# Performance work log

Hardware: AMD Instinct MI355X
Metric: run time of the kernel (lower is better)

Reference implementation:

```python
import jax, jax.numpy as jnp
import numpy as np

N = 10000      # nodes
E = 160000     # edges
F_IN = 128     # input_dim
HID = 128      # hidden_dim = per-head channels (concat=False)
OUT = 128      # output_dim
H = 4          # heads
L = 4          # layers (all 128->128 here, so params stack)


def setup_inputs() -> dict:
    key = jax.random.key(0)
    ks = jax.random.split(key, 12)
    x = jax.random.normal(ks[0], (N, F_IN), dtype=jnp.float32)
    edge_index = jax.random.randint(ks[1], (2, E), 0, N, dtype=jnp.int64)
    s = 1.0 / np.sqrt(F_IN)
    Wq = jax.random.normal(ks[2], (L, F_IN, H * HID), dtype=jnp.float32) * s
    bq = jnp.zeros((L, H * HID), dtype=jnp.float32)
    Wk = jax.random.normal(ks[3], (L, F_IN, H * HID), dtype=jnp.float32) * s
    bk = jnp.zeros((L, H * HID), dtype=jnp.float32)
    Wv = jax.random.normal(ks[4], (L, F_IN, H * HID), dtype=jnp.float32) * s
    bv = jnp.zeros((L, H * HID), dtype=jnp.float32)
    Wskip = jax.random.normal(ks[5], (L, F_IN, HID), dtype=jnp.float32) * s
    bskip = jnp.zeros((L, HID), dtype=jnp.float32)
    return {"x": x, "edge_index": edge_index, "Wq": Wq, "bq": bq,
            "Wk": Wk, "bk": bk, "Wv": Wv, "bv": bv,
            "Wskip": Wskip, "bskip": bskip}


def _transformer_conv(x, src, dst, Wq, bq, Wk, bk, Wv, bv, Ws, bs):
    # PyG TransformerConv, concat=False (mean over heads), root_weight=True
    n = x.shape[0]
    q = (x @ Wq + bq).reshape(n, H, HID)
    k = (x @ Wk + bk).reshape(n, H, HID)
    v = (x @ Wv + bv).reshape(n, H, HID)
    # per-edge attention logits: [E, H]
    alpha = jnp.einsum('ehc,ehc->eh', q[dst], k[src]) / jnp.sqrt(jnp.float32(HID))
    # segment softmax over destination node
    m = jax.ops.segment_max(alpha, dst, num_segments=n)          # [N, H]
    e = jnp.exp(alpha - m[dst])                                  # [E, H]
    z = jax.ops.segment_sum(e, dst, num_segments=n)              # [N, H]
    a = e / z[dst]                                               # [E, H]
    msg = a[:, :, None] * v[src]                                 # [E, H, C]
    out = jax.ops.segment_sum(msg, dst, num_segments=n)          # [N, H, C]
    out = out.mean(axis=1)                                       # concat=False
    return out + x @ Ws + bs                                     # skip (root_weight)


def reference(x, edge_index, Wq, bq, Wk, bk, Wv, bv, Wskip, bskip):
    src = edge_index[0]
    dst = edge_index[1]
    h = x
    for l in range(L - 1):
        h = _transformer_conv(h, src, dst, Wq[l], bq[l], Wk[l], bk[l],
                              Wv[l], bv[l], Wskip[l], bskip[l])
        h = jax.nn.relu(h)  # dropout p in eval/reference is identity
    h = _transformer_conv(h, src, dst, Wq[-1], bq[-1], Wk[-1], bk[-1],
                          Wv[-1], bv[-1], Wskip[-1], bskip[-1])
    return h
```

## Files before the change

### kernel.cpp

```cpp
#include <hip/hip_runtime.h>
#include <math.h>

static constexpr int F  = 128;
static constexpr int H  = 4;
static constexpr int HF = 512;
static constexpr int NCP = 640;
static constexpr int LAYERS = 4;

typedef __attribute__((ext_vector_type(8))) short bf16x8;
typedef __attribute__((ext_vector_type(4))) float f32x4;

__device__ __forceinline__ unsigned short f2bf(float f) {
    union { float f; unsigned u; } v; v.f = f;
    unsigned r = (v.u + 0x7FFFu + ((v.u >> 16) & 1u)) >> 16;
    return (unsigned short)r;
}
__device__ __forceinline__ float bf2f(unsigned short b) {
    union { unsigned u; float f; } v; v.u = ((unsigned)b) << 16;
    return v.f;
}

__device__ __forceinline__ float row16_sum(float x) {
    int t;
    t = __builtin_amdgcn_update_dpp(0, __float_as_int(x), 0xB1, 0xF, 0xF, true);
    x += __int_as_float(t);
    t = __builtin_amdgcn_update_dpp(0, __float_as_int(x), 0x4E, 0xF, 0xF, true);
    x += __int_as_float(t);
    t = __builtin_amdgcn_update_dpp(0, __float_as_int(x), 0x124, 0xF, 0xF, true);
    x += __int_as_float(t);
    t = __builtin_amdgcn_update_dpp(0, __float_as_int(x), 0x128, 0xF, 0xF, true);
    x += __int_as_float(t);
    return x;
}

__global__ void zero_kernel(int* __restrict__ p, int n) {
    int i = blockIdx.x * blockDim.x + threadIdx.x;
    if (i < n) p[i] = 0;
}

__global__ void hist_kernel(const int* __restrict__ dst, int* __restrict__ deg, int E) {
    int e = blockIdx.x * blockDim.x + threadIdx.x;
    if (e < E) atomicAdd(&deg[dst[e]], 1);
}

__global__ void scan_kernel(const int* __restrict__ deg, int* __restrict__ row_ptr, int n) {
    __shared__ int wsum[16];
    __shared__ int carry_s, wtot_s;
    const int tid = threadIdx.x;
    const int lane = tid & 63;
    const int wid = tid >> 6;
    if (tid == 0) { carry_s = 0; row_ptr[0] = 0; }
    __syncthreads();
    for (int base = 0; base < n; base += 1024) {
        int i = base + tid;
        int x = (i < n) ? deg[i] : 0;
#pragma unroll
        for (int off = 1; off < 64; off <<= 1) {
            int t = __shfl_up(x, off, 64);
            if (lane >= off) x += t;
        }
        if (lane == 63) wsum[wid] = x;
        __syncthreads();
        if (tid == 0) {
            int s = 0;
#pragma unroll
            for (int j = 0; j < 16; ++j) { int t = wsum[j]; wsum[j] = s; s += t; }
            wtot_s = s;
        }
        __syncthreads();
        int incl = x + wsum[wid] + carry_s;
        if (i < n) row_ptr[i + 1] = incl;
        __syncthreads();
        if (tid == 0) carry_s += wtot_s;
        __syncthreads();
    }
}

__global__ void scatter_kernel(const int* __restrict__ src, const int* __restrict__ dst,
                               const int* __restrict__ row_ptr, int* __restrict__ cursor,
                               int* __restrict__ csr_src, int E) {
    int e = blockIdx.x * blockDim.x + threadIdx.x;
    if (e < E) {
        int d = dst[e];
        int pos = atomicAdd(&cursor[d], 1);
        csr_src[row_ptr[d] + pos] = src[e];
    }
}

static constexpr int NB_CONV  = 1250;
static constexpr int NB_WQK   = 64;
static constexpr int NB_WS    = 64;
static constexpr int NB_BPOST = 256;
static constexpr int NB_BIAS  = LAYERS;
static constexpr int NB_PREP  = NB_CONV + NB_WQK + NB_WS + NB_BPOST + NB_BIAS;

__global__ __launch_bounds__(256) void prep_kernel(
    const float* __restrict__ x, unsigned short* __restrict__ h_bf, int n4,
    const float* __restrict__ Wq, const float* __restrict__ Wk,
    const float* __restrict__ Wv, const float* __restrict__ Ws,
    const float* __restrict__ bq, const float* __restrict__ bs, const float* __restrict__ bv,
    unsigned short* __restrict__ Bpre, unsigned short* __restrict__ Bpost,
    float* __restrict__ biasPre, float* __restrict__ biasPost, float scale)
{
    __shared__ __attribute__((aligned(16))) float smem[64 * 33 * 2];
    const int tid = threadIdx.x;
    int b = blockIdx.x;

    if (b < NB_CONV) {
        int i = b * 256 + tid;
        if (i < n4) {
            float4 v = *(const float4*)(x + (size_t)i * 4);
            ushort4 o;
            o.x = f2bf(v.x); o.y = f2bf(v.y); o.z = f2bf(v.z); o.w = f2bf(v.w);
            *(ushort4*)(h_bf + (size_t)i * 4) = o;
        }
        return;
    }
    b -= NB_CONV;
    if (b < NB_WQK) {
        float (*As)[33] = (float (*)[33])smem;
        float (*Bs)[33] = (float (*)[33])(smem + 64 * 33);
        const int bx = b & 1, by = (b >> 1) & 1, lh = b >> 2;
        const int l = lh >> 2, h = lh & 3;
        const int c0 = by * 64, k0 = bx * 64;
        const float* Ab = Wk + (size_t)l * 65536 + h * 128;
        const float* Bb = Wq + (size_t)l * 65536 + h * 128;
        const int tx = tid & 15, ty = tid >> 4;
        float acc[4][4] = {};
        for (int jj = 0; jj < 128; jj += 32) {
#pragma unroll
            for (int rep = 0; rep < 2; ++rep) {
                int f = tid + rep * 256;
                int r = f >> 3, j4 = (f & 7) * 4;
                float4 a = *(const float4*)(Ab + (size_t)(c0 + r) * 512 + jj + j4);
                As[r][j4 + 0] = a.x; As[r][j4 + 1] = a.y; As[r][j4 + 2] = a.z; As[r][j4 + 3] = a.w;
                float4 bb = *(const float4*)(Bb + (size_t)(k0 + r) * 512 + jj + j4);
                Bs[r][j4 + 0] = bb.x; Bs[r][j4 + 1] = bb.y; Bs[r][j4 + 2] = bb.z; Bs[r][j4 + 3] = bb.w;
            }
            __syncthreads();
#pragma unroll
            for (int j = 0; j < 32; ++j) {
                float a0 = As[ty * 4 + 0][j], a1 = As[ty * 4 + 1][j];
                float a2 = As[ty * 4 + 2][j], a3 = As[ty * 4 + 3][j];
                float b0 = Bs[tx * 4 + 0][j], b1 = Bs[tx * 4 + 1][j];
                float b2 = Bs[tx * 4 + 2][j], b3 = Bs[tx * 4 + 3][j];
                acc[0][0] += a0 * b0; acc[0][1] += a0 * b1; acc[0][2] += a0 * b2; acc[0][3] += a0 * b3;
                acc[1][0] += a1 * b0; acc[1][1] += a1 * b1; acc[1][2] += a1 * b2; acc[1][3] += a1 * b3;
                acc[2][0] += a2 * b0; acc[2][1] += a2 * b1; acc[2][2] += a2 * b2; acc[2][3] += a2 * b3;
                acc[3][0] += a3 * b0; acc[3][1] += a3 * b1; acc[3][2] += a3 * b2; acc[3][3] += a3 * b3;
            }
            __syncthreads();
        }
#pragma unroll
        for (int i = 0; i < 4; ++i)
#pragma unroll
            for (int t = 0; t < 4; ++t) {
                int c = c0 + ty * 4 + i;
                int k = k0 + tx * 4 + t;
                Bpre[(size_t)l * NCP * 128 + (size_t)(h * 128 + c) * 128 + k] = f2bf(scale * acc[i][t]);
            }
        return;
    }
    b -= NB_WQK;
    if (b < NB_WS) {
        unsigned short (*t)[33] = (unsigned short (*)[33])smem;
        const int bx = b & 3, by = (b >> 2) & 3, l = b >> 4;
        const int k0 = bx * 32, n0 = by * 32;
        const int cx = tid & 31, ry = tid >> 5;
#pragma unroll
        for (int rr = 0; rr < 32; rr += 8) {
            int k = k0 + ry + rr;
            t[ry + rr][cx] = f2bf(Ws[(size_t)l * 16384 + (size_t)k * 128 + n0 + cx]);
        }
        __syncthreads();
#pragma unroll
        for (int rr = 0; rr < 32; rr += 8) {
            int n = n0 + ry + rr;
            Bpre[(size_t)l * NCP * 128 + (size_t)(512 + n) * 128 + k0 + cx] = t[cx][ry + rr];
        }
        return;
    }
    b -= NB_WS;
    if (b < NB_BPOST) {
        unsigned short (*t)[33] = (unsigned short (*)[33])smem;
        const int bx = b & 3, by = (b >> 2) & 3, lh = b >> 4;
        const int l = lh >> 2, h = lh & 3;
        const int ci0 = bx * 32, co0 = by * 32;
        const int cx = tid & 31, ry = tid >> 5;
#pragma unroll
        for (int rr = 0; rr < 32; rr += 8) {
            int ci = ci0 + ry + rr;
            t[ry + rr][cx] = f2bf(0.25f * Wv[(size_t)l * 65536 + (size_t)ci * 512 + h * 128 + co0 + cx]);
        }
        __syncthreads();
#pragma unroll
        for (int rr = 0; rr < 32; rr += 8) {
            int co = co0 + ry + rr;
            Bpost[(size_t)l * 65536 + (size_t)co * 512 + h * 128 + ci0 + cx] = t[cx][ry + rr];
        }
        return;
    }
    b -= NB_BPOST;
    {
        const int l = b;
        for (int n = tid; n < 512; n += 256) {
            int h = n >> 7, c = n & 127;
            float s = 0.f;
            for (int j = 0; j < 128; ++j)
                s += bq[(size_t)l * 512 + h * 128 + j] * Wk[(size_t)l * 65536 + (size_t)c * 512 + h * 128 + j];
            biasPre[(size_t)l * NCP + n] = s * scale;
        }
        for (int c = tid; c < 128; c += 256) {
            float s = 0.f;
            for (int h = 0; h < 4; ++h) s += bv[(size_t)l * 512 + h * 128 + c];
            biasPost[(size_t)l * 128 + c] = 0.25f * s + bs[(size_t)l * 128 + c];
        }
    }
}

__global__ __launch_bounds__(256) void gemm_pre(
    const unsigned short* __restrict__ Abf,
    const unsigned short* __restrict__ Bt,
    const float* __restrict__ bias,
    unsigned short* __restrict__ Qt,
    int M)
{
    __shared__ unsigned short As[128][72];
    __shared__ unsigned short Bs[128][72];

    const int tid = threadIdx.x;
    const int wave = tid >> 6, lane = tid & 63;
    const int lane16 = lane & 15, quad = lane >> 4;
    const int wr = wave >> 1, wc = wave & 1;
    const int row0 = blockIdx.y * 128;
    const int col0 = blockIdx.x * 128;

    f32x4 acc[4][4] = {};

    for (int kk = 0; kk < 128; kk += 64) {
#pragma unroll
        for (int j = 0; j < 4; ++j) {
            int c = tid + j * 256;
            int r = c >> 3, c8 = (c & 7) * 8;
            bf16x8 v = {};
            if (row0 + r < M) v = *(const bf16x8*)(Abf + (size_t)(row0 + r) * 128 + kk + c8);
            *(bf16x8*)&As[r][c8] = v;
        }
#pragma unroll
        for (int j = 0; j < 4; ++j) {
            int c = tid + j * 256;
            int r = c >> 3, c8 = (c & 7) * 8;
            *(bf16x8*)&Bs[r][c8] = *(const bf16x8*)(Bt + (size_t)(col0 + r) * 128 + kk + c8);
        }
        __syncthreads();

#pragma unroll
        for (int ks = 0; ks < 2; ++ks) {
            bf16x8 a[4], b[4];
#pragma unroll
            for (int i = 0; i < 4; ++i)
                a[i] = *(const bf16x8*)&As[wr * 64 + i * 16 + lane16][ks * 32 + quad * 8];
#pragma unroll
            for (int i = 0; i < 4; ++i)
                b[i] = *(const bf16x8*)&Bs[wc * 64 + i * 16 + lane16][ks * 32 + quad * 8];
#pragma unroll
            for (int mi = 0; mi < 4; ++mi)
#pragma unroll
                for (int ni = 0; ni < 4; ++ni)
                    acc[mi][ni] = __builtin_amdgcn_mfma_f32_16x16x32_bf16(
                        a[mi], b[ni], acc[mi][ni], 0, 0, 0);
        }
        __syncthreads();
    }

#pragma unroll
    for (int mi = 0; mi < 4; ++mi) {
        int rowb = row0 + wr * 64 + mi * 16 + quad * 4;
#pragma unroll
        for (int ni = 0; ni < 4; ++ni) {
            int col = col0 + wc * 64 + ni * 16 + lane16;
            float bv = bias[col];
#pragma unroll
            for (int r = 0; r < 4; ++r) {
                int gr = rowb + r;
                if (gr < M) Qt[(size_t)gr * 512 + col] = f2bf(acc[mi][ni][r] + bv);
            }
        }
    }
}

__global__ __launch_bounds__(128, 4) void attn_agg(
    const unsigned short* __restrict__ Qt,
    const unsigned short* __restrict__ Hb,
    const int* __restrict__ row_ptr,
    const int* __restrict__ csr_src,
    unsigned short* __restrict__ Agg,
    int N)
{
    __shared__ float part[4][16][10];

    const int tid = threadIdx.x;
    const int wv  = tid >> 6;
    const int g   = (tid >> 4) & 3;
    const int l16 = tid & 15;
    const int node = blockIdx.x;

    const float NEG = -3e38f;

    float qf[8];
    {
        bf16x8 qv = *(const bf16x8*)(Qt + (size_t)node * HF + g * F + l16 * 8);
#pragma unroll
        for (int j = 0; j < 8; ++j) qf[j] = bf2f((unsigned short)qv[j]);
    }
    const unsigned short* Hl = Hb + (size_t)l16 * 8;

    const int beg = row_ptr[node];
    const int end = row_ptr[node + 1];

    float m = NEG, z = 0.f;
    float acc[8];
#pragma unroll
    for (int j = 0; j < 8; ++j) acc[j] = 0.f;

    const int begw = beg + wv * 4;
    if (begw < end) {
        const int last = end - 1;
        const int NB = (end - begw + 7) >> 3;

#define CLD(i) csr_src[(i) < last ? (i) : last]

        int a0 = CLD(begw + 0), a1 = CLD(begw + 1), a2 = CLD(begw + 2), a3 = CLD(begw + 3);
        bf16x8 hA0 = *(const bf16x8*)(Hl + (size_t)a0 * F);
        bf16x8 hA1 = *(const bf16x8*)(Hl + (size_t)a1 * F);
        bf16x8 hA2 = *(const bf16x8*)(Hl + (size_t)a2 * F);
        bf16x8 hA3 = *(const bf16x8*)(Hl + (size_t)a3 * F);
        int b0 = CLD(begw + 8), b1 = CLD(begw + 9), b2 = CLD(begw + 10), b3 = CLD(begw + 11);
        bf16x8 hB0 = *(const bf16x8*)(Hl + (size_t)b0 * F);
        bf16x8 hB1 = *(const bf16x8*)(Hl + (size_t)b1 * F);
        bf16x8 hB2 = *(const bf16x8*)(Hl + (size_t)b2 * F);
        bf16x8 hB3 = *(const bf16x8*)(Hl + (size_t)b3 * F);
        a0 = CLD(begw + 16); a1 = CLD(begw + 17); a2 = CLD(begw + 18); a3 = CLD(begw + 19);
        b0 = CLD(begw + 24); b1 = CLD(begw + 25); b2 = CLD(begw + 26); b3 = CLD(begw + 27);
        __builtin_amdgcn_sched_barrier(0);

#define ATTN_BATCH(H0, H1, H2, H3, I0, I1, I2, I3)                              \
    {                                                                           \
        float hf[4][8];                                                         \
        _Pragma("unroll")                                                       \
        for (int j = 0; j < 8; ++j) {                                           \
            hf[0][j] = bf2f((unsigned short)H0[j]);                             \
            hf[1][j] = bf2f((unsigned short)H1[j]);                             \
            hf[2][j] = bf2f((unsigned short)H2[j]);                             \
            hf[3][j] = bf2f((unsigned short)H3[j]);                             \
        }                                                                       \
        if (k + 2 < NB) {                                                       \
            H0 = *(const bf16x8*)(Hl + (size_t)I0 * F);                         \
            H1 = *(const bf16x8*)(Hl + (size_t)I1 * F);                         \
            H2 = *(const bf16x8*)(Hl + (size_t)I2 * F);                         \
            H3 = *(const bf16x8*)(Hl + (size_t)I3 * F);                         \
            I0 = CLD(base + 32); I1 = CLD(base + 33);                           \
            I2 = CLD(base + 34); I3 = CLD(base + 35);                           \
        }                                                                       \
        __builtin_amdgcn_sched_barrier(0);   \
        float p0 = 0.f, p1 = 0.f, p2 = 0.f, p3 = 0.f;                           \
        _Pragma("unroll")                                                       \
        for (int j = 0; j < 8; ++j) {                                           \
            p0 += qf[j] * hf[0][j]; p1 += qf[j] * hf[1][j];                     \
            p2 += qf[j] * hf[2][j]; p3 += qf[j] * hf[3][j];                     \
        }                                                                       \
        p0 = row16_sum(p0); p1 = row16_sum(p1);                                 \
        p2 = row16_sum(p2); p3 = row16_sum(p3);                                 \
        const int nv = end - base;                                              \
        if (nv < 4) { if (nv < 2) p1 = NEG; if (nv < 3) p2 = NEG; p3 = NEG; }   \
        float bm = fmaxf(fmaxf(p0, p1), fmaxf(p2, p3));                         \
        float mn = fmaxf(m, bm);                                                \
        float rs = exp2f(m - mn);                                               \
        float w0 = exp2f(p0 - mn), w1 = exp2f(p1 - mn);                         \
        float w2 = exp2f(p2 - mn), w3 = exp2f(p3 - mn);                         \
        z = z * rs + (w0 + w1) + (w2 + w3);                                     \
        _Pragma("unroll")                                                       \
        for (int j = 0; j < 8; ++j)                                             \
            acc[j] = acc[j] * rs + w0 * hf[0][j] + w1 * hf[1][j]                \
                   + w2 * hf[2][j] + w3 * hf[3][j];                             \
        m = mn;                                                                 \
    }

        int base = begw;
        int k = 0;
        for (;;) {
            ATTN_BATCH(hA0, hA1, hA2, hA3, a0, a1, a2, a3)
            ++k; base += 8;
            if (k >= NB) break;
            ATTN_BATCH(hB0, hB1, hB2, hB3, b0, b1, b2, b3)
            ++k; base += 8;
            if (k >= NB) break;
        }
#undef ATTN_BATCH
#undef CLD
    }

    if (wv == 1) {
#pragma unroll
        for (int j = 0; j < 8; ++j) part[g][l16][j] = acc[j];
        part[g][l16][8] = m;
        part[g][l16][9] = z;
    }
    __syncthreads();
    if (wv == 0) {
        float om = part[g][l16][8];
        float oz = part[g][l16][9];
        float M  = fmaxf(m, om);
        float sa = exp2f(m - M);
        float sb = exp2f(om - M);
        float zz = z * sa + oz * sb;
        float inv = (zz > 0.f) ? 1.f / zz : 0.f;
        bf16x8 o;
#pragma unroll
        for (int j = 0; j < 8; ++j)
            o[j] = (short)f2bf((acc[j] * sa + part[g][l16][j] * sb) * inv);
        *(bf16x8*)(Agg + (size_t)node * HF + g * F + l16 * 8) = o;
    }
}

__global__ __launch_bounds__(256) void gemm_post(
    const unsigned short* __restrict__ Agg,
    const unsigned short* __restrict__ Hc,
    const unsigned short* __restrict__ Bt,
    const unsigned short* __restrict__ Bsk,
    const float* __restrict__ bias,
    float* __restrict__ out_f,
    unsigned short* __restrict__ out_bf,
    int relu, int M)
{
    __shared__ unsigned short As[64][72];
    __shared__ unsigned short Bs[64][72];

    const int tid = threadIdx.x;
    const int wave = tid >> 6, lane = tid & 63;
    const int lane16 = lane & 15, quad = lane >> 4;
    const int row0 = blockIdx.y * 64;
    const int col0 = blockIdx.x * 64;

    f32x4 acc[4] = {};

    for (int kk = 0; kk < 640; kk += 64) {
        const bool sk = kk >= 512;
        const int k0 = sk ? kk - 512 : kk;
#pragma unroll
        for (int rep = 0; rep < 2; ++rep) {
            int c = tid + rep * 256;
            int r = c >> 3, c8 = (c & 7) * 8;
            bf16x8 v = {};
            if (row0 + r < M)
                v = sk ? *(const bf16x8*)(Hc  + (size_t)(row0 + r) * 128 + k0 + c8)
                       : *(const bf16x8*)(Agg + (size_t)(row0 + r) * 512 + k0 + c8);
            *(bf16x8*)&As[r][c8] = v;
            *(bf16x8*)&Bs[r][c8] = sk
                ? *(const bf16x8*)(Bsk + (size_t)(col0 + r) * 128 + k0 + c8)
                : *(const bf16x8*)(Bt  + (size_t)(col0 + r) * 512 + k0 + c8);
        }
        __syncthreads();

#pragma unroll
        for (int ks = 0; ks < 2; ++ks) {
            bf16x8 b = *(const bf16x8*)&Bs[wave * 16 + lane16][ks * 32 + quad * 8];
#pragma unroll
            for (int mt = 0; mt < 4; ++mt) {
                bf16x8 a = *(const bf16x8*)&As[mt * 16 + lane16][ks * 32 + quad * 8];
                acc[mt] = __builtin_amdgcn_mfma_f32_16x16x32_bf16(a, b, acc[mt], 0, 0, 0);
            }
        }
        __syncthreads();
    }

    const int col = col0 + wave * 16 + lane16;
    const float bcol = bias[col];
#pragma unroll
    for (int mt = 0; mt < 4; ++mt) {
#pragma unroll
        for (int r = 0; r < 4; ++r) {
            int row = row0 + mt * 16 + quad * 4 + r;
            if (row < M) {
                float v = acc[mt][r] + bcol;
                if (relu) v = fmaxf(v, 0.f);
                if (out_f)  out_f[(size_t)row * 128 + col] = v;
                if (out_bf) out_bf[(size_t)row * 128 + col] = f2bf(v);
            }
        }
    }
}

extern "C" void kernel_launch(void* const* d_in, const int* in_sizes, int n_in,
                              void* d_out, int out_size, void* d_ws, size_t ws_size,
                              hipStream_t stream) {
    const float* x     = (const float*)d_in[0];
    const int*   ei    = (const int*)d_in[1];
    const float* Wq    = (const float*)d_in[2];
    const float* bq    = (const float*)d_in[3];
    const float* Wk    = (const float*)d_in[4];
    const float* bk    = (const float*)d_in[5];
    const float* Wv    = (const float*)d_in[6];
    const float* bv    = (const float*)d_in[7];
    const float* Wskip = (const float*)d_in[8];
    const float* bskip = (const float*)d_in[9];
    float* out = (float*)d_out;
    (void)bk;

    const int N = in_sizes[0] / F;
    const int E = in_sizes[1] / 2;
    const float scale = 0.08838834764831845f * 1.4426950408889634f;

    const int* src = ei;
    const int* dst = ei + E;

    char* p = (char*)d_ws;
    float* biasPreP = (float*)p;               p += (size_t)LAYERS * NCP * sizeof(float);
    float* biasPostP= (float*)p;               p += (size_t)LAYERS * 128 * sizeof(float);
    unsigned short* h0    = (unsigned short*)p; p += (size_t)N * F * sizeof(unsigned short);
    unsigned short* h1    = (unsigned short*)p; p += (size_t)N * F * sizeof(unsigned short);
    unsigned short* Qt    = (unsigned short*)p; p += (size_t)N * HF * sizeof(unsigned short);
    unsigned short* AggB  = (unsigned short*)p; p += (size_t)N * HF * sizeof(unsigned short);
    unsigned short* BpreP = (unsigned short*)p; p += (size_t)LAYERS * NCP * 128 * sizeof(unsigned short);
    unsigned short* BpostP= (unsigned short*)p; p += (size_t)LAYERS * 128 * 512 * sizeof(unsigned short);
    int* deg     = (int*)p;                    p += (size_t)N * sizeof(int);
    int* cursor  = (int*)p;                    p += (size_t)N * sizeof(int);
    int* row_ptr = (int*)p;                    p += (size_t)(N + 1) * sizeof(int);
    int* csr_src = (int*)p;

    {
        int blocks = (E + 255) / 256;
        int zn = 2 * N;
        zero_kernel<<<(zn + 255) / 256, 256, 0, stream>>>(deg, zn);
        hist_kernel<<<blocks, 256, 0, stream>>>(dst, deg, E);
        scan_kernel<<<1, 1024, 0, stream>>>(deg, row_ptr, N);
        scatter_kernel<<<blocks, 256, 0, stream>>>(src, dst, row_ptr, cursor, csr_src, E);
    }

    prep_kernel<<<NB_PREP, 256, 0, stream>>>(x, h0, N * F / 4,
                                             Wq, Wk, Wv, Wskip,
                                             bq, bskip, bv,
                                             BpreP, BpostP, biasPreP, biasPostP, scale);

    const int rowBlocks128 = (N + 127) / 128;
    const int rowBlocks64  = (N + 63) / 64;

    unsigned short* hcur = h0;
    unsigned short* hnxt = h1;
    for (int l = 0; l < LAYERS; ++l) {
        dim3 gridPre(4, rowBlocks128);
        gemm_pre<<<gridPre, 256, 0, stream>>>(hcur,
                                              BpreP + (size_t)l * NCP * 128,
                                              biasPreP + (size_t)l * NCP,
                                              Qt, N);

        attn_agg<<<N, 128, 0, stream>>>(Qt, hcur, row_ptr, csr_src, AggB, N);

        float* out_f = nullptr;
        unsigned short* out_bf = nullptr;
        int relu;
        if (l == LAYERS - 1) { out_f = out; relu = 0; }
        else { out_bf = hnxt; relu = 1; }

        dim3 gridPost(2, rowBlocks64);
        gemm_post<<<gridPost, 256, 0, stream>>>(AggB, hcur,
                                                BpostP + (size_t)l * 128 * 512,
                                                BpreP + (size_t)l * NCP * 128 + (size_t)512 * 128,
                                                biasPostP + (size_t)l * 128,
                                                out_f, out_bf, relu, N);

        unsigned short* t = hcur; hcur = hnxt; hnxt = t;
    }
}
```

Measured before the change: 254.5 us.

## Fuse post-aggregation GEMM with next layer's Q projection GEMM

For non-final layers, a single kernel now computes the post-aggregation GEMM (agg plus skip, with ReLU), keeps the resulting 64-row tile of hidden states in shared memory, and immediately multiplies it by the next layer's 512-column Q weights. This drops one kernel launch per layer and the re-read of the hidden states from global memory. In exchange the fused grid has only about 157 blocks, each doing serial work over four column tiles, so parallelism drops compared with the separate 2D-gridded GEMMs.

```diff
diff --git a/kernel.cpp b/kernel.cpp
--- a/kernel.cpp
+++ b/kernel.cpp
@@ -423,15 +423,136 @@
     }
 }
 
+__global__ __launch_bounds__(256) void gemm_post_pre(
+    const unsigned short* __restrict__ Agg,
+    const unsigned short* __restrict__ Hc,
+    const unsigned short* __restrict__ BtPost,
+    const unsigned short* __restrict__ Bsk,
+    const float* __restrict__ biasPost,
+    unsigned short* __restrict__ Hn,
+    const unsigned short* __restrict__ BtPre,
+    const float* __restrict__ biasPre,
+    unsigned short* __restrict__ Qt,
+    int M)
+{
+    __shared__ unsigned short As[64][72];
+    __shared__ unsigned short Bs[128][72];
+    __shared__ unsigned short Hs[64][136];
+
+    const int tid = threadIdx.x;
+    const int wave = tid >> 6, lane = tid & 63;
+    const int lane16 = lane & 15, quad = lane >> 4;
+    const int row0 = blockIdx.x * 64;
+
+    {
+        f32x4 acc[4][2] = {};
+        for (int kk = 0; kk < 640; kk += 64) {
+            const bool sk = kk >= 512;
+            const int k0 = sk ? kk - 512 : kk;
+#pragma unroll
+            for (int j = 0; j < 2; ++j) {
+                int c = tid + j * 256;
+                int r = c >> 3, c8 = (c & 7) * 8;
+                bf16x8 v = {};
+                if (row0 + r < M)
+                    v = sk ? *(const bf16x8*)(Hc  + (size_t)(row0 + r) * 128 + k0 + c8)
+                           : *(const bf16x8*)(Agg + (size_t)(row0 + r) * 512 + k0 + c8);
+                *(bf16x8*)&As[r][c8] = v;
+            }
+#pragma unroll
+            for (int j = 0; j < 4; ++j) {
+                int c = tid + j * 256;
+                int r = c >> 3, c8 = (c & 7) * 8;
+                *(bf16x8*)&Bs[r][c8] = sk
+                    ? *(const bf16x8*)(Bsk    + (size_t)r * 128 + k0 + c8)
+                    : *(const bf16x8*)(BtPost + (size_t)r * 512 + k0 + c8);
+            }
+            __syncthreads();
+#pragma unroll
+            for (int ks = 0; ks < 2; ++ks) {
+                bf16x8 b[2];
+#pragma unroll
+                for (int ni = 0; ni < 2; ++ni)
+                    b[ni] = *(const bf16x8*)&Bs[wave * 32 + ni * 16 + lane16][ks * 32 + quad * 8];
+#pragma unroll
+                for (int mi = 0; mi < 4; ++mi) {
+                    bf16x8 a = *(const bf16x8*)&As[mi * 16 + lane16][ks * 32 + quad * 8];
+#pragma unroll
+                    for (int ni = 0; ni < 2; ++ni)
+                        acc[mi][ni] = __builtin_amdgcn_mfma_f32_16x16x32_bf16(
+                            a, b[ni], acc[mi][ni], 0, 0, 0);
+                }
+            }
+            __syncthreads();
+        }
+#pragma unroll
+        for (int mi = 0; mi < 4; ++mi)
+#pragma unroll
+            for (int ni = 0; ni < 2; ++ni) {
+                int col = wave * 32 + ni * 16 + lane16;
+                float bcol = biasPost[col];
+#pragma unroll
+                for (int r = 0; r < 4; ++r) {
+                    int lr = mi * 16 + quad * 4 + r;
+                    unsigned short hb = f2bf(fmaxf(acc[mi][ni][r] + bcol, 0.f));
+                    Hs[lr][col] = hb;
+                    if (row0 + lr < M) Hn[(size_t)(row0 + lr) * 128 + col] = hb;
+                }
+            }
+    }
+    __syncthreads();
+
+    for (int ct = 0; ct < 4; ++ct) {
+        const int colp = ct * 128;
+        f32x4 acc2[4][2] = {};
+        for (int kk2 = 0; kk2 < 128; kk2 += 64) {
+#pragma unroll
+            for (int j = 0; j < 4; ++j) {
+                int c = tid + j * 256;
+                int r = c >> 3, c8 = (c & 7) * 8;
+                *(bf16x8*)&Bs[r][c8] =
+                    *(const bf16x8*)(BtPre + (size_t)(colp + r) * 128 + kk2 + c8);
+            }
+            __syncthreads();
+#pragma unroll
+            for (int ks = 0; ks < 2; ++ks) {
+                bf16x8 b[2];
+#pragma unroll
+                for (int ni = 0; ni < 2; ++ni)
+                    b[ni] = *(const bf16x8*)&Bs[wave * 32 + ni * 16 + lane16][ks * 32 + quad * 8];
+#pragma unroll
+                for (int mi = 0; mi < 4; ++mi) {
+                    bf16x8 a = *(const bf16x8*)&Hs[mi * 16 + lane16][kk2 + ks * 32 + quad * 8];
+#pragma unroll
+                    for (int ni = 0; ni < 2; ++ni)
+                        acc2[mi][ni] = __builtin_amdgcn_mfma_f32_16x16x32_bf16(
+                            a, b[ni], acc2[mi][ni], 0, 0, 0);
+                }
+            }
+            __syncthreads();
+        }
+#pragma unroll
+        for (int mi = 0; mi < 4; ++mi)
+#pragma unroll
+            for (int ni = 0; ni < 2; ++ni) {
+                int col = colp + wave * 32 + ni * 16 + lane16;
+                float bv = biasPre[col];
+#pragma unroll
+                for (int r = 0; r < 4; ++r) {
+                    int row = row0 + mi * 16 + quad * 4 + r;
+                    if (row < M) Qt[(size_t)row * 512 + col] = f2bf(acc2[mi][ni][r] + bv);
+                }
+            }
+    }
+}
+
 __global__ __launch_bounds__(256) void gemm_post(
     const unsigned short* __restrict__ Agg,
     const unsigned short* __restrict__ Hc,
     const unsigned short* __restrict__ Bt,
     const unsigned short* __restrict__ Bsk,
     const float* __restrict__ bias,
-    float* __restrict__ out_f,
-    unsigned short* __restrict__ out_bf,
-    int relu, int M)
+    float* __restrict__ out_f, int M)
 {
     __shared__ unsigned short As[64][72];
     __shared__ unsigned short Bs[64][72];
@@ -481,12 +602,7 @@
 #pragma unroll
         for (int r = 0; r < 4; ++r) {
             int row = row0 + mt * 16 + quad * 4 + r;
-            if (row < M) {
-                float v = acc[mt][r] + bcol;
-                if (relu) v = fmaxf(v, 0.f);
-                if (out_f)  out_f[(size_t)row * 128 + col] = v;
-                if (out_bf) out_bf[(size_t)row * 128 + col] = f2bf(v);
-            }
+            if (row < M) out_f[(size_t)row * 128 + col] = acc[mt][r] + bcol;
         }
     }
 }
@@ -547,28 +663,32 @@
 
     unsigned short* hcur = h0;
     unsigned short* hnxt = h1;
+
+    dim3 gridPre(4, rowBlocks128);
+    gemm_pre<<<gridPre, 256, 0, stream>>>(hcur, BpreP, biasPreP, Qt, N);
+
     for (int l = 0; l < LAYERS; ++l) {
-        dim3 gridPre(4, rowBlocks128);
-        gemm_pre<<<gridPre, 256, 0, stream>>>(hcur,
-                                              BpreP + (size_t)l * NCP * 128,
-                                              biasPreP + (size_t)l * NCP,
-                                              Qt, N);
-
         attn_agg<<<N, 128, 0, stream>>>(Qt, hcur, row_ptr, csr_src, AggB, N);
 
-        float* out_f = nullptr;
-        unsigned short* out_bf = nullptr;
-        int relu;
-        if (l == LAYERS - 1) { out_f = out; relu = 0; }
-        else { out_bf = hnxt; relu = 1; }
-
-        dim3 gridPost(2, rowBlocks64);
-        gemm_post<<<gridPost, 256, 0, stream>>>(AggB, hcur,
-                                                BpostP + (size_t)l * 128 * 512,
-                                                BpreP + (size_t)l * NCP * 128 + (size_t)512 * 128,
-                                                biasPostP + (size_t)l * 128,
-                                                out_f, out_bf, relu, N);
-
-        unsigned short* t = hcur; hcur = hnxt; hnxt = t;
-    }
-}
+        if (l < LAYERS - 1) {
+            gemm_post_pre<<<rowBlocks64, 256, 0, stream>>>(
+                AggB, hcur,
+                BpostP + (size_t)l * 128 * 512,
+                BpreP + (size_t)l * NCP * 128 + (size_t)512 * 128,
+                biasPostP + (size_t)l * 128,
+                hnxt,
+                BpreP + (size_t)(l + 1) * NCP * 128,
+                biasPreP + (size_t)(l + 1) * NCP,
+                Qt, N);
+            unsigned short* t = hcur; hcur = hnxt; hnxt = t;
+        } else {
+            dim3 gridPost(2, rowBlocks64);
+            gemm_post<<<gridPost, 256, 0, stream>>>(
+                AggB, hcur,
+                BpostP + (size_t)l * 128 * 512,
+                BpreP + (size_t)l * NCP * 128 + (size_t)512 * 128,
+                biasPostP + (size_t)l * 128,
+                out, N);
+        }
+    }
+}
```

Result: slower. 266.6 us (+4.8%).
